# Kernel optimization log

Hardware: AMD Instinct MI355X
Metric: run time of the kernel (lower is better)

The kernel has to match this reference:

```python
import jax, jax.numpy as jnp
import numpy as np

B, S, D, U = 32, 2048, 512, 512

def setup_inputs() -> dict:
    key = jax.random.key(0)
    k1, k2, k3, k4, k5 = jax.random.split(key, 5)
    passage = jax.random.normal(k1, (B, S, D), dtype=jnp.float32)
    hidden = jax.random.normal(k2, (B, D), dtype=jnp.float32)
    mask = jnp.ones((B, S), dtype=jnp.float32)
    # learned params (Dense kernels, glorot-ish scale)
    W1 = jax.random.normal(k3, (D, U), dtype=jnp.float32) / np.sqrt(D)
    W2 = jax.random.normal(k4, (D, U), dtype=jnp.float32) / np.sqrt(D)
    Vw = jax.random.normal(k5, (U, 1), dtype=jnp.float32) / np.sqrt(U)
    Vb = jnp.zeros((1,), dtype=jnp.float32)
    return {"passage": passage, "hidden": hidden, "mask": mask,
            "W1": W1, "W2": W2, "Vw": Vw, "Vb": Vb}

def reference(passage, hidden, mask, W1, W2, Vw, Vb):
    # passage: [B,S,D], hidden: [B,D], mask: [B,S]
    h_proj = jnp.einsum('bd,du->bu', hidden, W2)[:, None, :]        # [B,1,U]
    p_proj = jnp.einsum('bsd,du->bsu', passage, W1)                  # [B,S,U]
    score = jnp.einsum('bsu,uo->bso', jnp.tanh(p_proj + h_proj), Vw) + Vb  # [B,S,1]
    score = score + ((1.0 - mask) * -1e30)[:, :, None]
    attention_weights = jax.nn.softmax(score, axis=1)                # [B,S,1]
    context_vector = jnp.sum(attention_weights * passage, axis=1)    # [B,D]
    return context_vector, attention_weights
```

## Files before the change

### kernel.cpp

```cpp
#include <hip/hip_runtime.h>
#include <hip/hip_bf16.h>
#include <cstddef>


#define NB 32
#define NS 2048
#define ND 512
#define NU 512

typedef __bf16 bf16_t;
typedef __bf16 bf16x8 __attribute__((ext_vector_type(8)));
typedef float floatx4 __attribute__((ext_vector_type(4)));

__global__ __launch_bounds__(256) void prep_kernel(
    const float* __restrict__ W1, bf16_t* __restrict__ W1p,
    const float* __restrict__ hidden, const float* __restrict__ W2,
    float* __restrict__ hproj) {
    if (blockIdx.x < 1024) {
        int idx = blockIdx.x * 256 + threadIdx.x;
        int k = idx >> 9, n = idx & 511;
        int kc = k >> 5, q = (k >> 3) & 3, jj = k & 7;
        int ng = n >> 4, c = n & 15;
        int dst = (((kc << 5) + ng) << 9) + (q << 7) + (c << 3) + jj;
        W1p[dst] = (bf16_t)W1[idx];
    } else {
        __shared__ float h[ND];
        __shared__ float part[256];
        int bi = blockIdx.x - 1024;
        int b = bi >> 2, ug = bi & 3;
        int t = threadIdx.x;
        h[t] = hidden[b * ND + t];
        h[t + 256] = hidden[b * ND + t + 256];
        __syncthreads();
        int u = (ug << 7) + (t & 127);
        int d0 = (t >> 7) << 8;
        float acc = 0.f;
#pragma unroll 8
        for (int d = d0; d < d0 + 256; ++d) acc = fmaf(h[d], W2[d * NU + u], acc);
        part[t] = acc;
        __syncthreads();
        if (t < 128) hproj[b * NU + u] = part[t] + part[t + 128];
    }
}

__global__ __launch_bounds__(512, 4) void score_kernel(
    const float* __restrict__ passage, const bf16_t* __restrict__ W1p,
    const float* __restrict__ hproj, const float* __restrict__ Vw,
    const float* __restrict__ Vb, float* __restrict__ scores) {
    __shared__ bf16_t Asf[64 * 512];
    const int tid = threadIdx.x;
    const int wave = tid >> 6, lane = tid & 63;
    const int q = lane >> 4, c = lane & 15;
    const int m0 = blockIdx.x * 64;
    const int b = m0 >> 11;

#pragma unroll
    for (int it = 0; it < 8; ++it) {
        int idx = it * 512 + tid;
        int row = idx >> 6, c8 = idx & 63;
        const float4* src = (const float4*)(passage + ((size_t)(m0 + row) << 9)) + (c8 << 1);
        float4 v0 = src[0], v1 = src[1];
        bf16x8 w;
        w[0] = (bf16_t)v0.x; w[1] = (bf16_t)v0.y; w[2] = (bf16_t)v0.z; w[3] = (bf16_t)v0.w;
        w[4] = (bf16_t)v1.x; w[5] = (bf16_t)v1.y; w[6] = (bf16_t)v1.z; w[7] = (bf16_t)v1.w;
        ((bf16x8*)(Asf + (row << 9)))[c8 ^ (row & 7)] = w;
    }
    __syncthreads();

    floatx4 acc[4][4];
#pragma unroll
    for (int i = 0; i < 4; ++i)
#pragma unroll
        for (int j = 0; j < 4; ++j) { floatx4 z = {0.f, 0.f, 0.f, 0.f}; acc[i][j] = z; }

    const bf16x8* Wq = (const bf16x8*)W1p;
    const int ng0 = wave << 2;

    for (int kc = 0; kc < 16; ++kc) {
        bf16x8 a[4], bb[4];
        int chunk = (kc << 2) + q;
#pragma unroll
        for (int i = 0; i < 4; ++i)
            a[i] = ((const bf16x8*)(Asf + ((i * 16 + c) << 9)))[chunk ^ (c & 7)];
#pragma unroll
        for (int j = 0; j < 4; ++j)
            bb[j] = Wq[(((kc << 5) + ng0 + j) << 6) + lane];
#pragma unroll
        for (int j = 0; j < 4; ++j)
#pragma unroll
            for (int i = 0; i < 4; ++i)
                acc[i][j] = __builtin_amdgcn_mfma_f32_16x16x32_bf16(a[i], bb[j], acc[i][j], 0, 0, 0);
    }

    float sp[4][4];
#pragma unroll
    for (int i = 0; i < 4; ++i)
#pragma unroll
        for (int r = 0; r < 4; ++r) sp[i][r] = 0.f;
#pragma unroll
    for (int j = 0; j < 4; ++j) {
        int n = (wave << 6) + (j << 4) + c;
        float hp = hproj[(b << 9) + n];
        float vw = Vw[n];
#pragma unroll
        for (int i = 0; i < 4; ++i)
#pragma unroll
            for (int r = 0; r < 4; ++r) {
                float x = acc[i][j][r] + hp;
                float e = __expf(2.0f * x);
                float t = 1.0f - 2.0f * __builtin_amdgcn_rcpf(e + 1.0f);
                sp[i][r] = fmaf(t, vw, sp[i][r]);
            }
    }
#pragma unroll
    for (int off = 1; off < 16; off <<= 1)
#pragma unroll
        for (int i = 0; i < 4; ++i)
#pragma unroll
            for (int r = 0; r < 4; ++r)
                sp[i][r] += __shfl_xor(sp[i][r], off, 64);

    __syncthreads();
    float* red = (float*)Asf;
    if (c == 0) {
#pragma unroll
        for (int i = 0; i < 4; ++i)
#pragma unroll
            for (int r = 0; r < 4; ++r)
                red[wave * 64 + i * 16 + q * 4 + r] = sp[i][r];
    }
    __syncthreads();
    if (tid < 64) {
        float s = Vb[0];
#pragma unroll
        for (int w = 0; w < 8; ++w) s += red[w * 64 + tid];
        scores[m0 + tid] = s;
    }
}

__global__ __launch_bounds__(1024) void softmax_kernel(
    const float* __restrict__ mask, float* __restrict__ attn) {
    __shared__ float smx[16], ssm[16];
    int b = blockIdx.x, tid = threadIdx.x;
    int wave = tid >> 6, lane = tid & 63;
    const int base = b * NS;
    float v0 = attn[base + tid] + (1.0f - mask[base + tid]) * (-1e30f);
    float v1 = attn[base + 1024 + tid] + (1.0f - mask[base + 1024 + tid]) * (-1e30f);
    float mx = fmaxf(v0, v1);
#pragma unroll
    for (int off = 1; off < 64; off <<= 1) mx = fmaxf(mx, __shfl_xor(mx, off, 64));
    if (lane == 0) smx[wave] = mx;
    __syncthreads();
    mx = smx[0];
#pragma unroll
    for (int w = 1; w < 16; ++w) mx = fmaxf(mx, smx[w]);
    v0 = __expf(v0 - mx); v1 = __expf(v1 - mx);
    float sum = v0 + v1;
#pragma unroll
    for (int off = 1; off < 64; off <<= 1) sum += __shfl_xor(sum, off, 64);
    if (lane == 0) ssm[wave] = sum;
    __syncthreads();
    sum = 0.f;
#pragma unroll
    for (int w = 0; w < 16; ++w) sum += ssm[w];
    float inv = 1.0f / sum;
    attn[base + tid] = v0 * inv;
    attn[base + 1024 + tid] = v1 * inv;
}

__global__ __launch_bounds__(256) void context_kernel(
    const float* __restrict__ passage, const float* __restrict__ attn,
    float* __restrict__ ctx) {
    __shared__ float4 part[256];
    int bb = blockIdx.x >> 5, sc = blockIdx.x & 31, t = threadIdx.x;
    int col = t & 127, half = t >> 7;
    const float4* p = (const float4*)(passage + (((size_t)bb * NS + sc * 64 + half * 32) << 9));
    const float* wp = attn + bb * NS + sc * 64 + half * 32;
    float ax = 0.f, ay = 0.f, az = 0.f, aw = 0.f;
#pragma unroll 8
    for (int s = 0; s < 32; ++s) {
        float w = wp[s];
        float4 v = p[(size_t)s * 128 + col];
        ax = fmaf(w, v.x, ax); ay = fmaf(w, v.y, ay);
        az = fmaf(w, v.z, az); aw = fmaf(w, v.w, aw);
    }
    float4 mine; mine.x = ax; mine.y = ay; mine.z = az; mine.w = aw;
    part[t] = mine;
    __syncthreads();
    if (t < 128) {
        float4 o = part[t + 128];
        float* dst = ctx + bb * ND + t * 4;
        atomicAdd(dst + 0, ax + o.x); atomicAdd(dst + 1, ay + o.y);
        atomicAdd(dst + 2, az + o.z); atomicAdd(dst + 3, aw + o.w);
    }
}

extern "C" void kernel_launch(void* const* d_in, const int* in_sizes, int n_in,
                              void* d_out, int out_size, void* d_ws, size_t ws_size,
                              hipStream_t stream) {
    const float* passage = (const float*)d_in[0];
    const float* hidden  = (const float*)d_in[1];
    const float* mask    = (const float*)d_in[2];
    const float* W1      = (const float*)d_in[3];
    const float* W2      = (const float*)d_in[4];
    const float* Vw      = (const float*)d_in[5];
    const float* Vb      = (const float*)d_in[6];

    float* ctx  = (float*)d_out;
    float* attn = (float*)d_out + NB * ND;

    bf16_t* W1p  = (bf16_t*)d_ws;
    float* hproj = (float*)((char*)d_ws + (size_t)NU * ND * 2);

    hipMemsetAsync(ctx, 0, (size_t)NB * ND * sizeof(float), stream);
    prep_kernel<<<dim3(1024 + 128), dim3(256), 0, stream>>>(W1, W1p, hidden, W2, hproj);
    score_kernel<<<dim3(NB * NS / 64), dim3(512), 0, stream>>>(passage, W1p, hproj, Vw, Vb, attn);
    softmax_kernel<<<dim3(NB), dim3(1024), 0, stream>>>(mask, attn);
    context_kernel<<<dim3(NB * 32), dim3(256), 0, stream>>>(passage, attn, ctx);
}
```

Baseline: 272.0 us.

## Double-buffer passage K-slices in score kernel and widen context blocks

The score kernel now stages the 64-row passage tile in four K-slices of 128 columns, held in two padded LDS buffers. The next slice's global loads are issued before the MFMAs on the current slice, replacing the single up-front load of the whole tile. This is meant to overlap HBM reads and fp32-to-bf16 conversion with matrix math, and it shrinks LDS use. It adds a barrier per slice and lowers the launch-bounds occupancy hint from 4 to 3. The context kernel uses 512 threads, so each thread handles 16 rows instead of 32, giving more memory parallelism per block at the cost of a larger shared reduction.

```diff
diff --git a/kernel.cpp b/kernel.cpp
--- a/kernel.cpp
+++ b/kernel.cpp
@@ -11,6 +11,9 @@
 typedef __bf16 bf16_t;
 typedef __bf16 bf16x8 __attribute__((ext_vector_type(8)));
 typedef float floatx4 __attribute__((ext_vector_type(4)));
+
+#define ROWP 136
+#define SLICE (64 * ROWP)
 
 __global__ __launch_bounds__(256) void prep_kernel(
     const float* __restrict__ W1, bf16_t* __restrict__ W1p,
@@ -43,27 +46,38 @@
     }
 }
 
-__global__ __launch_bounds__(512, 4) void score_kernel(
+__global__ __launch_bounds__(512, 3) void score_kernel(
     const float* __restrict__ passage, const bf16_t* __restrict__ W1p,
     const float* __restrict__ hproj, const float* __restrict__ Vw,
     const float* __restrict__ Vb, float* __restrict__ scores) {
-    __shared__ bf16_t Asf[64 * 512];
+    __shared__ bf16_t Asf[2 * SLICE];
     const int tid = threadIdx.x;
     const int wave = tid >> 6, lane = tid & 63;
     const int q = lane >> 4, c = lane & 15;
     const int m0 = blockIdx.x * 64;
     const int b = m0 >> 11;
-
-#pragma unroll
-    for (int it = 0; it < 8; ++it) {
-        int idx = it * 512 + tid;
-        int row = idx >> 6, c8 = idx & 63;
-        const float4* src = (const float4*)(passage + ((size_t)(m0 + row) << 9)) + (c8 << 1);
-        float4 v0 = src[0], v1 = src[1];
-        bf16x8 w;
-        w[0] = (bf16_t)v0.x; w[1] = (bf16_t)v0.y; w[2] = (bf16_t)v0.z; w[3] = (bf16_t)v0.w;
-        w[4] = (bf16_t)v1.x; w[5] = (bf16_t)v1.y; w[6] = (bf16_t)v1.z; w[7] = (bf16_t)v1.w;
-        ((bf16x8*)(Asf + (row << 9)))[c8 ^ (row & 7)] = w;
+    const int ng0 = wave << 2;
+    const bf16x8* Wq = (const bf16x8*)W1p;
+
+    const int srow = tid >> 3, skp = tid & 7;
+    const float4* sbase = (const float4*)(passage + ((size_t)(m0 + srow) << 9)) + (skp << 2);
+    const int swoff = srow * ROWP + (skp << 4);
+
+#define CVT_WRITE(dst, v0, v1, v2, v3) {                                     \
+    bf16x8 w0, w1;                                                           \
+    w0[0] = (bf16_t)(v0).x; w0[1] = (bf16_t)(v0).y;                          \
+    w0[2] = (bf16_t)(v0).z; w0[3] = (bf16_t)(v0).w;                          \
+    w0[4] = (bf16_t)(v1).x; w0[5] = (bf16_t)(v1).y;                          \
+    w0[6] = (bf16_t)(v1).z; w0[7] = (bf16_t)(v1).w;                          \
+    w1[0] = (bf16_t)(v2).x; w1[1] = (bf16_t)(v2).y;                          \
+    w1[2] = (bf16_t)(v2).z; w1[3] = (bf16_t)(v2).w;                          \
+    w1[4] = (bf16_t)(v3).x; w1[5] = (bf16_t)(v3).y;                          \
+    w1[6] = (bf16_t)(v3).z; w1[7] = (bf16_t)(v3).w;                          \
+    *(bf16x8*)(dst) = w0; *(bf16x8*)((dst) + 8) = w1; }
+
+    {
+        float4 v0 = sbase[0], v1 = sbase[1], v2 = sbase[2], v3 = sbase[3];
+        CVT_WRITE(Asf + swoff, v0, v1, v2, v3);
     }
     __syncthreads();
 
@@ -73,24 +87,36 @@
 #pragma unroll
         for (int j = 0; j < 4; ++j) { floatx4 z = {0.f, 0.f, 0.f, 0.f}; acc[i][j] = z; }
 
-    const bf16x8* Wq = (const bf16x8*)W1p;
-    const int ng0 = wave << 2;
-
-    for (int kc = 0; kc < 16; ++kc) {
-        bf16x8 a[4], bb[4];
-        int chunk = (kc << 2) + q;
-#pragma unroll
-        for (int i = 0; i < 4; ++i)
-            a[i] = ((const bf16x8*)(Asf + ((i * 16 + c) << 9)))[chunk ^ (c & 7)];
-#pragma unroll
-        for (int j = 0; j < 4; ++j)
-            bb[j] = Wq[(((kc << 5) + ng0 + j) << 6) + lane];
-#pragma unroll
-        for (int j = 0; j < 4; ++j)
+    for (int sl = 0; sl < 4; ++sl) {
+        float4 p0, p1, p2, p3;
+        if (sl < 3) {
+            const float4* nb = sbase + ((sl + 1) << 5);
+            p0 = nb[0]; p1 = nb[1]; p2 = nb[2]; p3 = nb[3];
+        }
+        const bf16_t* Ab = Asf + (sl & 1) * SLICE;
+#pragma unroll
+        for (int kcl = 0; kcl < 4; ++kcl) {
+            int kc = (sl << 2) + kcl;
+            bf16x8 a[4], bb[4];
 #pragma unroll
             for (int i = 0; i < 4; ++i)
-                acc[i][j] = __builtin_amdgcn_mfma_f32_16x16x32_bf16(a[i], bb[j], acc[i][j], 0, 0, 0);
-    }
+                a[i] = *(const bf16x8*)(Ab + (i * 16 + c) * ROWP + (((kcl << 2) + q) << 3));
+#pragma unroll
+            for (int j = 0; j < 4; ++j)
+                bb[j] = Wq[(((kc << 5) + ng0 + j) << 6) + lane];
+#pragma unroll
+            for (int j = 0; j < 4; ++j)
+#pragma unroll
+                for (int i = 0; i < 4; ++i)
+                    acc[i][j] = __builtin_amdgcn_mfma_f32_16x16x32_bf16(a[i], bb[j], acc[i][j], 0, 0, 0);
+        }
+        if (sl < 3) {
+            bf16_t* wr = Asf + ((sl + 1) & 1) * SLICE + swoff;
+            CVT_WRITE(wr, p0, p1, p2, p3);
+        }
+        __syncthreads();
+    }
+#undef CVT_WRITE
 
     float sp[4][4];
 #pragma unroll
@@ -120,7 +146,6 @@
             for (int r = 0; r < 4; ++r)
                 sp[i][r] += __shfl_xor(sp[i][r], off, 64);
 
-    __syncthreads();
     float* red = (float*)Asf;
     if (c == 0) {
 #pragma unroll
@@ -168,17 +193,17 @@
     attn[base + 1024 + tid] = v1 * inv;
 }
 
-__global__ __launch_bounds__(256) void context_kernel(
+__global__ __launch_bounds__(512) void context_kernel(
     const float* __restrict__ passage, const float* __restrict__ attn,
     float* __restrict__ ctx) {
-    __shared__ float4 part[256];
+    __shared__ float4 part[512];
     int bb = blockIdx.x >> 5, sc = blockIdx.x & 31, t = threadIdx.x;
-    int col = t & 127, half = t >> 7;
-    const float4* p = (const float4*)(passage + (((size_t)bb * NS + sc * 64 + half * 32) << 9));
-    const float* wp = attn + bb * NS + sc * 64 + half * 32;
+    int col = t & 127, qh = t >> 7;
+    const float4* p = (const float4*)(passage + (((size_t)bb * NS + sc * 64 + qh * 16) << 9));
+    const float* wp = attn + bb * NS + sc * 64 + qh * 16;
     float ax = 0.f, ay = 0.f, az = 0.f, aw = 0.f;
-#pragma unroll 8
-    for (int s = 0; s < 32; ++s) {
+#pragma unroll 16
+    for (int s = 0; s < 16; ++s) {
         float w = wp[s];
         float4 v = p[(size_t)s * 128 + col];
         ax = fmaf(w, v.x, ax); ay = fmaf(w, v.y, ay);
@@ -188,10 +213,12 @@
     part[t] = mine;
     __syncthreads();
     if (t < 128) {
-        float4 o = part[t + 128];
+        float4 o1 = part[t + 128], o2 = part[t + 256], o3 = part[t + 384];
         float* dst = ctx + bb * ND + t * 4;
-        atomicAdd(dst + 0, ax + o.x); atomicAdd(dst + 1, ay + o.y);
-        atomicAdd(dst + 2, az + o.z); atomicAdd(dst + 3, aw + o.w);
+        atomicAdd(dst + 0, ax + o1.x + o2.x + o3.x);
+        atomicAdd(dst + 1, ay + o1.y + o2.y + o3.y);
+        atomicAdd(dst + 2, az + o1.z + o2.z + o3.z);
+        atomicAdd(dst + 3, aw + o1.w + o2.w + o3.w);
     }
 }
 
@@ -216,5 +243,5 @@
     prep_kernel<<<dim3(1024 + 128), dim3(256), 0, stream>>>(W1, W1p, hidden, W2, hproj);
     score_kernel<<<dim3(NB * NS / 64), dim3(512), 0, stream>>>(passage, W1p, hproj, Vw, Vb, attn);
     softmax_kernel<<<dim3(NB), dim3(1024), 0, stream>>>(mask, attn);
-    context_kernel<<<dim3(NB * 32), dim3(256), 0, stream>>>(passage, attn, ctx);
-}
+    context_kernel<<<dim3(NB * 32), dim3(512), 0, stream>>>(passage, attn, ctx);
+}
```

Measured after the change: 306.1 us. +12.6%, slower.

## Prefetch W1 tiles two steps ahead, vectorize W1 pack, widen context blocks

Applied to the files above, without the earlier changes.

The score kernel now loads B-operand (W1p) fragments two k-chunks ahead into registers, issuing the first two before the passage staging loop so global latency overlaps with MFMA work, and fully unrolls the k loop. The W1 packing in the prep kernel has each lane gather eight values and emit one bf16x8 vector store instead of scattered scalar stores, cutting its block count. The context kernel uses 512 threads with four 16-row slices per block to raise memory-level parallelism. Register pressure rises in the score kernel, which could hurt occupancy under the 512x4 launch bounds.

```diff
diff --git a/kernel.cpp b/kernel.cpp
--- a/kernel.cpp
+++ b/kernel.cpp
@@ -16,17 +16,20 @@
     const float* __restrict__ W1, bf16_t* __restrict__ W1p,
     const float* __restrict__ hidden, const float* __restrict__ W2,
     float* __restrict__ hproj) {
-    if (blockIdx.x < 1024) {
-        int idx = blockIdx.x * 256 + threadIdx.x;
-        int k = idx >> 9, n = idx & 511;
-        int kc = k >> 5, q = (k >> 3) & 3, jj = k & 7;
-        int ng = n >> 4, c = n & 15;
-        int dst = (((kc << 5) + ng) << 9) + (q << 7) + (c << 3) + jj;
-        W1p[dst] = (bf16_t)W1[idx];
+    if (blockIdx.x < 128) {
+        int wave = threadIdx.x >> 6, lane = threadIdx.x & 63;
+        int f = (blockIdx.x << 2) + wave;
+        int kc = f >> 5, ng = f & 31;
+        int q = lane >> 4, c = lane & 15;
+        const float* src = W1 + (kc * 32 + q * 8) * 512 + ng * 16 + c;
+        bf16x8 w;
+#pragma unroll
+        for (int jj = 0; jj < 8; ++jj) w[jj] = (bf16_t)src[jj * 512];
+        ((bf16x8*)W1p)[(f << 6) + lane] = w;
     } else {
         __shared__ float h[ND];
         __shared__ float part[256];
-        int bi = blockIdx.x - 1024;
+        int bi = blockIdx.x - 128;
         int b = bi >> 2, ug = bi & 3;
         int t = threadIdx.x;
         h[t] = hidden[b * ND + t];
@@ -53,6 +56,17 @@
     const int q = lane >> 4, c = lane & 15;
     const int m0 = blockIdx.x * 64;
     const int b = m0 >> 11;
+    const int ng0 = wave << 2;
+    const bf16x8* Wq = (const bf16x8*)W1p;
+
+#define LOAD_B(dst, kc_) {                                                   \
+    _Pragma("unroll")                                                        \
+    for (int j = 0; j < 4; ++j)                                              \
+        dst[j] = Wq[((((kc_) << 5) + ng0 + j) << 6) + lane]; }
+
+    bf16x8 b0[4], b1[4];
+    LOAD_B(b0, 0);
+    LOAD_B(b1, 1);
 
 #pragma unroll
     for (int it = 0; it < 8; ++it) {
@@ -73,24 +87,24 @@
 #pragma unroll
         for (int j = 0; j < 4; ++j) { floatx4 z = {0.f, 0.f, 0.f, 0.f}; acc[i][j] = z; }
 
-    const bf16x8* Wq = (const bf16x8*)W1p;
-    const int ng0 = wave << 2;
-
+#pragma unroll
     for (int kc = 0; kc < 16; ++kc) {
-        bf16x8 a[4], bb[4];
+        bf16x8 bn[4];
+        if (kc < 14) LOAD_B(bn, kc + 2);
+        bf16x8 a[4];
         int chunk = (kc << 2) + q;
 #pragma unroll
         for (int i = 0; i < 4; ++i)
             a[i] = ((const bf16x8*)(Asf + ((i * 16 + c) << 9)))[chunk ^ (c & 7)];
 #pragma unroll
         for (int j = 0; j < 4; ++j)
-            bb[j] = Wq[(((kc << 5) + ng0 + j) << 6) + lane];
-#pragma unroll
-        for (int j = 0; j < 4; ++j)
 #pragma unroll
             for (int i = 0; i < 4; ++i)
-                acc[i][j] = __builtin_amdgcn_mfma_f32_16x16x32_bf16(a[i], bb[j], acc[i][j], 0, 0, 0);
-    }
+                acc[i][j] = __builtin_amdgcn_mfma_f32_16x16x32_bf16(a[i], b0[j], acc[i][j], 0, 0, 0);
+#pragma unroll
+        for (int j = 0; j < 4; ++j) { b0[j] = b1[j]; b1[j] = bn[j]; }
+    }
+#undef LOAD_B
 
     float sp[4][4];
 #pragma unroll
@@ -168,17 +182,17 @@
     attn[base + 1024 + tid] = v1 * inv;
 }
 
-__global__ __launch_bounds__(256) void context_kernel(
+__global__ __launch_bounds__(512) void context_kernel(
     const float* __restrict__ passage, const float* __restrict__ attn,
     float* __restrict__ ctx) {
-    __shared__ float4 part[256];
+    __shared__ float4 part[512];
     int bb = blockIdx.x >> 5, sc = blockIdx.x & 31, t = threadIdx.x;
-    int col = t & 127, half = t >> 7;
-    const float4* p = (const float4*)(passage + (((size_t)bb * NS + sc * 64 + half * 32) << 9));
-    const float* wp = attn + bb * NS + sc * 64 + half * 32;
+    int col = t & 127, qh = t >> 7;
+    const float4* p = (const float4*)(passage + (((size_t)bb * NS + sc * 64 + qh * 16) << 9));
+    const float* wp = attn + bb * NS + sc * 64 + qh * 16;
     float ax = 0.f, ay = 0.f, az = 0.f, aw = 0.f;
-#pragma unroll 8
-    for (int s = 0; s < 32; ++s) {
+#pragma unroll 16
+    for (int s = 0; s < 16; ++s) {
         float w = wp[s];
         float4 v = p[(size_t)s * 128 + col];
         ax = fmaf(w, v.x, ax); ay = fmaf(w, v.y, ay);
@@ -188,10 +202,12 @@
     part[t] = mine;
     __syncthreads();
     if (t < 128) {
-        float4 o = part[t + 128];
+        float4 o1 = part[t + 128], o2 = part[t + 256], o3 = part[t + 384];
         float* dst = ctx + bb * ND + t * 4;
-        atomicAdd(dst + 0, ax + o.x); atomicAdd(dst + 1, ay + o.y);
-        atomicAdd(dst + 2, az + o.z); atomicAdd(dst + 3, aw + o.w);
+        atomicAdd(dst + 0, ax + o1.x + o2.x + o3.x);
+        atomicAdd(dst + 1, ay + o1.y + o2.y + o3.y);
+        atomicAdd(dst + 2, az + o1.z + o2.z + o3.z);
+        atomicAdd(dst + 3, aw + o1.w + o2.w + o3.w);
     }
 }
 
@@ -213,8 +229,8 @@
     float* hproj = (float*)((char*)d_ws + (size_t)NU * ND * 2);
 
     hipMemsetAsync(ctx, 0, (size_t)NB * ND * sizeof(float), stream);
-    prep_kernel<<<dim3(1024 + 128), dim3(256), 0, stream>>>(W1, W1p, hidden, W2, hproj);
+    prep_kernel<<<dim3(256), dim3(256), 0, stream>>>(W1, W1p, hidden, W2, hproj);
     score_kernel<<<dim3(NB * NS / 64), dim3(512), 0, stream>>>(passage, W1p, hproj, Vw, Vb, attn);
     softmax_kernel<<<dim3(NB), dim3(1024), 0, stream>>>(mask, attn);
-    context_kernel<<<dim3(NB * 32), dim3(256), 0, stream>>>(passage, attn, ctx);
-}
+    context_kernel<<<dim3(NB * 32), dim3(512), 0, stream>>>(passage, attn, ctx);
+}
```

Result: slower. 288.2 us (+6.0%).
